# Kernel optimization log

Measured on AMD Instinct MI355X. Metric: run time of the kernel, lower is better.

The kernel has to match this reference:

```python
import jax, jax.numpy as jnp
import numpy as np

DIM = 128; D_STATE = 16; D_CONV = 4; EXPAND = 2
D_INNER = DIM * EXPAND            # 256
DT_RANK = (DIM + 15) // 16        # 8
B, H, W = 2, 56, 56


def _ln(x, w, b):
    m = jnp.mean(x, -1, keepdims=True)
    v = jnp.var(x, -1, keepdims=True)
    return (x - m) * jax.lax.rsqrt(v + 1e-5) * w + b


def _mamba(x, in_w, conv_w, conv_b, xproj_w, dt_w, dt_b, A_log, Dp, out_w):
    # x: (B, L, DIM)
    Bb, L, _ = x.shape
    xz = x @ in_w.T                                   # (B,L,2*D_INNER)
    xi, z = jnp.split(xz, 2, axis=-1)
    # causal depthwise conv1d (pad left d_conv-1, truncate to L)
    xc = jnp.transpose(xi, (0, 2, 1))                 # (B,D_INNER,L)
    xc = jax.lax.conv_general_dilated(
        xc, conv_w, (1,), [(D_CONV - 1, 0)],
        dimension_numbers=('NCH', 'OIH', 'NCH'),
        feature_group_count=D_INNER) + conv_b[None, :, None]
    xs = jax.nn.silu(jnp.transpose(xc, (0, 2, 1)))    # (B,L,D_INNER)
    dbl = xs @ xproj_w.T                              # (B,L,DT_RANK+2*D_STATE)
    dt = jax.nn.softplus(dbl[..., :DT_RANK] @ dt_w.T + dt_b)   # (B,L,D_INNER)
    Bc = dbl[..., DT_RANK:DT_RANK + D_STATE]          # (B,L,D_STATE)
    Cc = dbl[..., DT_RANK + D_STATE:]                 # (B,L,D_STATE)
    A = -jnp.exp(A_log)                               # (D_INNER,D_STATE)
    dA = jnp.exp(dt[..., None] * A)                   # (B,L,D_INNER,D_STATE)
    dBu = (dt * xs)[..., None] * Bc[:, :, None, :]    # (B,L,D_INNER,D_STATE)

    def step(h, inp):
        a, bu, c = inp
        h = a * h + bu                                # (B,D_INNER,D_STATE)
        return h, jnp.einsum('bdn,bn->bd', h, c)

    h0 = jnp.zeros((Bb, D_INNER, D_STATE), x.dtype)
    _, ys = jax.lax.scan(step, h0, (jnp.moveaxis(dA, 1, 0),
                                    jnp.moveaxis(dBu, 1, 0),
                                    jnp.moveaxis(Cc, 1, 0)))
    y = jnp.moveaxis(ys, 0, 1) + xs * Dp              # (B,L,D_INNER)
    y = y * jax.nn.silu(z)
    return y @ out_w.T                                # (B,L,DIM)


def _forward(x, norm_h_w, norm_h_b, norm_v_w, norm_v_b,
             dw_w, dw_b, pw_w, pw_b,
             h_in_w, h_conv_w, h_conv_b, h_xproj_w, h_dt_w, h_dt_b, h_A_log, h_D, h_out_w,
             v_in_w, v_conv_w, v_conv_b, v_xproj_w, v_dt_w, v_dt_b, v_A_log, v_D, v_out_w,
             ca_fc1_w, ca_fc2_w):
    Bb, C, Hh, Ww = x.shape
    # local branch: depthwise 3x3 + GELU + 1x1
    lf = jax.lax.conv_general_dilated(
        x, dw_w, (1, 1), [(1, 1), (1, 1)],
        dimension_numbers=('NCHW', 'OIHW', 'NCHW'),
        feature_group_count=C) + dw_b[None, :, None, None]
    lf = jax.nn.gelu(lf, approximate=False)
    lf = jnp.einsum('bchw,oc->bohw', lf, pw_w[:, :, 0, 0]) + pw_b[None, :, None, None]
    # horizontal scan: row-major tokens
    xh = _ln(x.reshape(Bb, C, Hh * Ww).transpose(0, 2, 1), norm_h_w, norm_h_b)
    oh = _mamba(xh, h_in_w, h_conv_w, h_conv_b, h_xproj_w, h_dt_w, h_dt_b,
                h_A_log, h_D, h_out_w)
    oh = oh.transpose(0, 2, 1).reshape(Bb, C, Hh, Ww)
    # vertical scan: column-major tokens
    xv = _ln(jnp.transpose(x, (0, 1, 3, 2)).reshape(Bb, C, Ww * Hh).transpose(0, 2, 1),
             norm_v_w, norm_v_b)
    ov = _mamba(xv, v_in_w, v_conv_w, v_conv_b, v_xproj_w, v_dt_w, v_dt_b,
                v_A_log, v_D, v_out_w)
    ov = jnp.transpose(ov.transpose(0, 2, 1).reshape(Bb, C, Ww, Hh), (0, 1, 3, 2))
    fused = oh + ov + lf
    # channel attention
    y = jnp.mean(fused, axis=(2, 3))                  # (B,C)
    y = jax.nn.sigmoid(jax.nn.relu(y @ ca_fc1_w.T) @ ca_fc2_w.T)
    return fused * y[:, :, None, None] + x


def setup_inputs() -> dict:
    key = jax.random.key(0)
    ks = iter(jax.random.split(key, 64))
    def nrm(shape, scale):
        return jax.random.normal(next(ks), shape, jnp.float32) * scale
    d = {}
    d['x'] = nrm((B, DIM, H, W), 1.0)
    d['norm_h_w'] = jnp.ones((DIM,), jnp.float32); d['norm_h_b'] = jnp.zeros((DIM,), jnp.float32)
    d['norm_v_w'] = jnp.ones((DIM,), jnp.float32); d['norm_v_b'] = jnp.zeros((DIM,), jnp.float32)
    d['dw_w'] = nrm((DIM, 1, 3, 3), 1.0 / 3.0)
    d['dw_b'] = jnp.zeros((DIM,), jnp.float32)
    d['pw_w'] = nrm((DIM, DIM, 1, 1), DIM ** -0.5)
    d['pw_b'] = jnp.zeros((DIM,), jnp.float32)
    for p in ('h', 'v'):
        d[p + '_in_w'] = nrm((2 * D_INNER, DIM), DIM ** -0.5)
        d[p + '_conv_w'] = nrm((D_INNER, 1, D_CONV), D_CONV ** -0.5)
        d[p + '_conv_b'] = jnp.zeros((D_INNER,), jnp.float32)
        d[p + '_xproj_w'] = nrm((DT_RANK + 2 * D_STATE, D_INNER), D_INNER ** -0.5)
        d[p + '_dt_w'] = nrm((D_INNER, DT_RANK), DT_RANK ** -0.5)
        d[p + '_dt_b'] = jnp.full((D_INNER,), -2.0, jnp.float32)  # small positive dt
        d[p + '_A_log'] = jnp.log(jnp.tile(jnp.arange(1, D_STATE + 1, dtype=jnp.float32), (D_INNER, 1)))
        d[p + '_D'] = jnp.ones((D_INNER,), jnp.float32)
        d[p + '_out_w'] = nrm((DIM, D_INNER), D_INNER ** -0.5)
    d['ca_fc1_w'] = nrm((DIM // 4, DIM), DIM ** -0.5)
    d['ca_fc2_w'] = nrm((DIM, DIM // 4), (DIM // 4) ** -0.5)
    return d


def reference(x, norm_h_w, norm_h_b, norm_v_w, norm_v_b,
              dw_w, dw_b, pw_w, pw_b,
              h_in_w, h_conv_w, h_conv_b, h_xproj_w, h_dt_w, h_dt_b, h_A_log, h_D, h_out_w,
              v_in_w, v_conv_w, v_conv_b, v_xproj_w, v_dt_w, v_dt_b, v_A_log, v_D, v_out_w,
              ca_fc1_w, ca_fc2_w):
    return _forward(x, norm_h_w, norm_h_b, norm_v_w, norm_v_b,
                    dw_w, dw_b, pw_w, pw_b,
                    h_in_w, h_conv_w, h_conv_b, h_xproj_w, h_dt_w, h_dt_b, h_A_log, h_D, h_out_w,
                    v_in_w, v_conv_w, v_conv_b, v_xproj_w, v_dt_w, v_dt_b, v_A_log, v_D, v_out_w,
                    ca_fc1_w, ca_fc2_w)
```

## Files before the change

kernel.cpp:

```cpp
#include <hip/hip_runtime.h>
#include <hip/hip_bf16.h>

typedef __hip_bfloat16 bf16;
__device__ __forceinline__ float b2f(bf16 v){ return __bfloat162float(v); }
__device__ __forceinline__ bf16 f2b(float v){ return __float2bfloat16(v); }

typedef __attribute__((ext_vector_type(8))) short frag_ab;
typedef __attribute__((ext_vector_type(4))) float frag_cd;
typedef __attribute__((ext_vector_type(4))) short short4v;

__device__ __forceinline__ frag_ab ld_frag_2xb64(const bf16* p){
  union { frag_ab f; short4v h[2]; } u;
  u.h[0] = *reinterpret_cast<const short4v*>(p);
  u.h[1] = *reinterpret_cast<const short4v*>(p+4);
  return u.f;
}

__device__ __forceinline__ void st_agent(float* p, float v){
  __hip_atomic_store(p, v, __ATOMIC_RELAXED, __HIP_MEMORY_SCOPE_AGENT);
}
__device__ __forceinline__ float ld_agent(const float* p){
  return __hip_atomic_load(p, __ATOMIC_RELAXED, __HIP_MEMORY_SCOPE_AGENT);
}

#define LLEN 3136
#define BATCH 2
#define NCHUNK 49
#define LC 64

__global__ void k_front(const float* __restrict__ x, const float* __restrict__ dww,
                        const float* __restrict__ dwb, bf16* __restrict__ tmp,
                        const float* nhw_, const float* nhb_, const float* nvw_,
                        const float* nvb_, bf16* __restrict__ xln,
                        float* __restrict__ YMEAN, int* __restrict__ ZCNT,
                        const float* __restrict__ h_inw, const float* __restrict__ v_inw,
                        const float* __restrict__ h_ow,  const float* __restrict__ v_ow,
                        const float* __restrict__ pww,   const float* __restrict__ h_xw,
                        const float* __restrict__ v_xw,
                        bf16* __restrict__ WBIN, bf16* __restrict__ WBOUT,
                        bf16* __restrict__ WBPW, bf16* __restrict__ WBX){
  int blk = blockIdx.x;
  int tid = threadIdx.x;
  if (blk < 1024){
    int bc = blk & 255;
    int seg = blk >> 8;
    int c = bc & 127;
    if (blk == 0){
      if (tid < 256) YMEAN[tid] = 0.f;
      if (tid < 4)   ZCNT[tid] = 0;
    }
    const float* xp = x + (size_t)bc*LLEN;
    __shared__ float sxr[16][60];
    int r0 = seg*14;
    for (int idx = tid; idx < 16*56; idx += 256){
      int rr = idx/56, cc = idx%56;
      int gr = r0 - 1 + rr;
      sxr[rr][cc+1] = (gr >= 0 && gr < 56) ? xp[gr*56+cc] : 0.f;
    }
    if (tid < 16){ sxr[tid][0] = 0.f; sxr[tid][57] = 0.f; }
    float w[9];
    #pragma unroll
    for (int i=0;i<9;i++) w[i] = dww[c*9+i];
    float bias = dwb[c];
    __syncthreads();
    int pstart = seg * 784;
    for (int p = pstart + tid; p < pstart + 784; p += 256){
      int i = p/56, j = p%56;
      int li = i - r0;
      float acc = bias;
      #pragma unroll
      for (int a=0;a<3;a++)
        #pragma unroll
        for (int bb=0;bb<3;bb++)
          acc += w[a*3+bb] * sxr[li+a][j+bb];
      float g = 0.5f*acc*(1.0f + erff(acc*0.70710678118654752f));
      tmp[(size_t)bc*LLEN + p] = f2b(g);
    }
  } else if (blk < 1136){
    int idx2 = blk - 1024;
    int h = idx2 % 56, b = idx2 / 56;
    __shared__ float sx[128][57];
    __shared__ float smean[56], srstd[56];
    __shared__ float wh[128], bh[128], wv_[128], bv_[128];
    if (tid < 128){ wh[tid]=nhw_[tid]; bh[tid]=nhb_[tid];
                    wv_[tid]=nvw_[tid]; bv_[tid]=nvb_[tid]; }
    for (int idx = tid; idx < 128*56; idx += 256){
      int c = idx / 56, w = idx % 56;
      sx[c][w] = x[((size_t)(b*128+c))*LLEN + h*56 + w];
    }
    __syncthreads();
    if (tid < 56){
      float s=0.f, s2=0.f;
      for (int c=0;c<128;c++){ float v = sx[c][tid]; s+=v; s2+=v*v; }
      float m = s*(1.f/128.f);
      float var = s2*(1.f/128.f) - m*m;
      smean[tid]=m; srstd[tid]=rsqrtf(var+1e-5f);
    }
    __syncthreads();
    bf16* outh = xln;
    bf16* outv = xln + (size_t)BATCH*LLEN*128;
    for (int idx = tid; idx < 56*128; idx += 256){
      int w = idx >> 7, c = idx & 127;
      float v = (sx[c][w]-smean[w])*srstd[w];
      outh[((size_t)b*LLEN + h*56 + w)*128 + c] = f2b(v*wh[c]+bh[c]);
      outv[((size_t)b*LLEN + w*56 + h)*128 + c] = f2b(v*wv_[c]+bv_[c]);
    }
  } else {
    int pblk = blk - 1136;
    int t16 = tid*16;
    if (pblk < 32){
      int g = pblk*4096 + t16;
      int dir = g >> 16, off = g & 65535;
      const float* src = (dir ? v_inw : h_inw) + off;
      bf16* dst = WBIN + g;
      #pragma unroll
      for (int r=0;r<4;r++){
        float4 w4 = *reinterpret_cast<const float4*>(src + r*4);
        bf16 t4[4] = {f2b(w4.x), f2b(w4.y), f2b(w4.z), f2b(w4.w)};
        *reinterpret_cast<double*>(dst + r*4) = *reinterpret_cast<double*>(t4);
      }
    } else if (pblk < 48){
      int g = (pblk-32)*4096 + t16;
      int dir = g >> 15, off = g & 32767;
      const float* src = (dir ? v_ow : h_ow) + off;
      bf16* dst = WBOUT + g;
      #pragma unroll
      for (int r=0;r<4;r++){
        float4 w4 = *reinterpret_cast<const float4*>(src + r*4);
        bf16 t4[4] = {f2b(w4.x), f2b(w4.y), f2b(w4.z), f2b(w4.w)};
        *reinterpret_cast<double*>(dst + r*4) = *reinterpret_cast<double*>(t4);
      }
    } else if (pblk < 52){
      int g = (pblk-48)*4096 + t16;
      const float* src = pww + g;
      bf16* dst = WBPW + g;
      #pragma unroll
      for (int r=0;r<4;r++){
        float4 w4 = *reinterpret_cast<const float4*>(src + r*4);
        bf16 t4[4] = {f2b(w4.x), f2b(w4.y), f2b(w4.z), f2b(w4.w)};
        *reinterpret_cast<double*>(dst + r*4) = *reinterpret_cast<double*>(t4);
      }
    } else if (pblk < 58){
      int g = (pblk-52)*4096 + t16;
      int dir = (g >= 12288) ? 1 : 0;
      int off = g - dir*12288;
      int rr = off >> 8, cc = off & 255;
      bf16* dst = WBX + g;
      if (rr < 40){
        const float* src = (dir ? v_xw : h_xw) + rr*256 + cc;
        #pragma unroll
        for (int r=0;r<4;r++){
          float4 w4 = *reinterpret_cast<const float4*>(src + r*4);
          bf16 t4[4] = {f2b(w4.x), f2b(w4.y), f2b(w4.z), f2b(w4.w)};
          *reinterpret_cast<double*>(dst + r*4) = *reinterpret_cast<double*>(t4);
        }
      } else {
        bf16 z4[4] = {f2b(0.f), f2b(0.f), f2b(0.f), f2b(0.f)};
        double zd = *reinterpret_cast<double*>(z4);
        #pragma unroll
        for (int r=0;r<4;r++) *reinterpret_cast<double*>(dst + r*4) = zd;
      }
    }
  }
}

__global__ void k_inproj(const bf16* __restrict__ xln, const bf16* __restrict__ WBIN,
                         bf16* __restrict__ XI, bf16* __restrict__ Z){
  int dir = blockIdx.z;
  const bf16* A = xln + (size_t)dir*BATCH*LLEN*128;
  const bf16* Wb = WBIN + (size_t)dir*512*128;
  int m0 = blockIdx.x*64;
  int npair = blockIdx.y*128;
  __shared__ __align__(16) bf16 sA[64][136];
  __shared__ __align__(16) bf16 sW[64][136];
  int tid = threadIdx.x;
  #pragma unroll
  for (int r=0;r<4;r++){
    int idx = tid + r*256;
    int row = idx >> 4, c8 = (idx & 15)*8;
    *reinterpret_cast<float4*>(&sA[row][c8]) =
        *reinterpret_cast<const float4*>(&A[(size_t)(m0+row)*128 + c8]);
  }
  int wv2 = tid >> 6, lane = tid & 63;
  int qd = lane >> 4, mr = lane & 15;
  bf16* dst = (npair < 256) ? XI : Z;
  int nbase0 = npair & 255;
  size_t dslab = (size_t)dir*BATCH*LLEN*256;
  #pragma unroll
  for (int nt=0; nt<2; nt++){
    int n0 = npair + nt*64;
    __syncthreads();
    #pragma unroll
    for (int r=0;r<4;r++){
      int idx = tid + r*256;
      int row = idx >> 4, c8 = (idx & 15)*8;
      *reinterpret_cast<float4*>(&sW[row][c8]) =
          *reinterpret_cast<const float4*>(&Wb[(size_t)(n0+row)*128 + c8]);
    }
    __syncthreads();
    frag_cd acc[4] = {};
    #pragma unroll
    for (int k0=0;k0<128;k0+=32){
      frag_ab af = *reinterpret_cast<frag_ab*>(&sA[wv2*16+mr][k0+qd*8]);
      #pragma unroll
      for (int t=0;t<4;t++){
        frag_ab bfr = *reinterpret_cast<frag_ab*>(&sW[t*16+mr][k0+qd*8]);
        acc[t] = __builtin_amdgcn_mfma_f32_16x16x32_bf16(af, bfr, acc[t], 0, 0, 0);
      }
    }
    int nb = nbase0 + nt*64;
    #pragma unroll
    for (int t=0;t<4;t++)
      #pragma unroll
      for (int r=0;r<4;r++){
        int row = m0 + wv2*16 + qd*4 + r;
        int col = nb + t*16 + mr;
        dst[dslab + (size_t)row*256 + col] = f2b(acc[t][r]);
      }
  }
}

__global__ void k_dbl(const bf16* __restrict__ XI,
                      const float* hcw, const float* hcb, const float* vcw, const float* vcb,
                      const bf16* __restrict__ WBX,
                      const float* hdw, const float* vdw, const float* hdb, const float* vdb,
                      bf16* __restrict__ XS2, bf16* __restrict__ DT2,
                      float* __restrict__ Bf, float* __restrict__ Cf){
  int m0 = blockIdx.x*64;
  int bd = m0 / LLEN;
  int l0m = m0 % LLEN;
  int dirq = bd >> 1;
  const bf16* XId = XI + (size_t)bd*LLEN*256;
  const bf16* Wb = WBX + (size_t)dirq*48*256;
  const float* cw = dirq ? vcw : hcw;
  const float* cb = dirq ? vcb : hcb;
  __shared__ __align__(16) bf16 sA[67][264];
  __shared__ __align__(16) bf16 sW[48][264];
  __shared__ float sdbl[64][49];
  int tid = threadIdx.x;
  for (int idx = tid; idx < 67*32; idx += 256){
    int row = idx >> 5, c8 = (idx & 31)*8;
    int l = l0m - 3 + row;
    float4 v = make_float4(0.f,0.f,0.f,0.f);
    if (l >= 0) v = *reinterpret_cast<const float4*>(&XId[(size_t)l*256 + c8]);
    *reinterpret_cast<float4*>(&sA[row][c8]) = v;
  }
  #pragma unroll
  for (int r=0;r<6;r++){
    int idx = tid + r*256;
    int row = idx >> 5, c8 = (idx & 31)*8;
    *reinterpret_cast<float4*>(&sW[row][c8]) =
        *reinterpret_cast<const float4*>(&Wb[(size_t)row*256 + c8]);
  }
  __syncthreads();
  {
    float w0=cw[tid*4], w1=cw[tid*4+1], w2=cw[tid*4+2], w3=cw[tid*4+3];
    float cbias = cb[tid];
    size_t x2base = ((size_t)bd*16 + (tid>>4))*LLEN + l0m;
    int c16 = tid & 15;
    float xm3 = b2f(sA[0][tid]), xm2 = b2f(sA[1][tid]), xm1 = b2f(sA[2][tid]);
    #pragma unroll 4
    for (int j=0;j<64;j++){
      float x0 = b2f(sA[j+3][tid]);
      float acc = cbias + w0*xm3 + w1*xm2 + w2*xm1 + w3*x0;
      float s = acc / (1.f + __expf(-acc));
      bf16 sv = f2b(s);
      sA[j][tid] = sv;
      XS2[(x2base + j)*16 + c16] = sv;
      xm3=xm2; xm2=xm1; xm1=x0;
    }
  }
  __syncthreads();
  int wv2 = tid >> 6, lane = tid & 63;
  int qd = lane >> 4, mr = lane & 15;
  frag_cd acc[3] = {};
  #pragma unroll
  for (int k0=0;k0<256;k0+=32){
    frag_ab af = *reinterpret_cast<frag_ab*>(&sA[wv2*16+mr][k0+qd*8]);
    #pragma unroll
    for (int t=0;t<3;t++){
      frag_ab bfr = *reinterpret_cast<frag_ab*>(&sW[t*16+mr][k0+qd*8]);
      acc[t] = __builtin_amdgcn_mfma_f32_16x16x32_bf16(af, bfr, acc[t], 0, 0, 0);
    }
  }
  #pragma unroll
  for (int t=0;t<3;t++)
    #pragma unroll
    for (int r=0;r<4;r++){
      int col = t*16 + mr;
      if (col < 40) sdbl[wv2*16 + qd*4 + r][col] = acc[t][r];
    }
  __syncthreads();
  const float* dtw = dirq ? vdw : hdw;
  const float* dtb = dirq ? vdb : hdb;
  float w8[8];
  #pragma unroll
  for (int r=0;r<8;r++) w8[r] = dtw[tid*8+r];
  float biasv = dtb[tid];
  size_t d2base = ((size_t)bd*16 + (tid>>4))*LLEN + l0m;
  int c16 = tid & 15;
  for (int row=0; row<64; row++){
    float a = biasv;
    #pragma unroll
    for (int r=0;r<8;r++) a += sdbl[row][r]*w8[r];
    float sv = (a > 20.f) ? a : __logf(1.f + __expf(a));
    DT2[(d2base + row)*16 + c16] = f2b(sv);
  }
  #pragma unroll
  for (int r=0;r<8;r++){
    int idx = tid + r*256;
    int row = idx >> 5, o = idx & 31;
    float v = sdbl[row][8+o];
    size_t rr = (size_t)(m0+row)*16;
    if (o < 16) Bf[rr + o] = v;
    else        Cf[rr + (o-16)] = v;
  }
}

__global__ void k_scan1(const bf16* __restrict__ DT2, const bf16* __restrict__ XS2,
                        const float* __restrict__ Bc, const float* hA, const float* vA,
                        float* __restrict__ Pbuf, float* __restrict__ Hbuf){
  int bd = blockIdx.z;
  int g  = blockIdx.y;
  int ck = blockIdx.x;
  int l0 = ck*LC;
  const float* Bd = Bc + (size_t)bd*LLEN*16;
  const float* Alog = (bd >> 1) ? vA : hA;
  int tid = threadIdx.x;
  int dl = tid >> 4, n = tid & 15;
  float A = -__expf(Alog[(g*16+dl)*16+n]);
  __shared__ float sdt[LC][16], sxs[LC][16], sB[LC][16];
  size_t base2 = (((size_t)bd*16 + g)*LLEN + l0)*16;
  #pragma unroll
  for (int r=0;r<4;r++){
    int idx = tid + r*256;
    sdt[idx>>4][idx&15] = b2f(DT2[base2 + idx]);
    sxs[idx>>4][idx&15] = b2f(XS2[base2 + idx]);
    (&sB[0][0])[idx] = Bd[(size_t)l0*16 + idx];
  }
  __syncthreads();
  float h = 0.f, P = 1.f;
  #pragma unroll 8
  for (int i=0;i<LC;i++){
    float a = sdt[i][dl];
    float u = sxs[i][dl];
    float dA = __expf(a * A);
    h = dA*h + (a*u)*sB[i][n];
    P *= dA;
  }
  size_t sidx = (((size_t)bd*16 + g)*NCHUNK + ck)*256 + tid;
  Pbuf[sidx] = P;
  Hbuf[sidx] = h;
}

__global__ void k_scan2(const float* __restrict__ Pbuf, float* __restrict__ Hbuf){
  int q = blockIdx.x;
  int tid = threadIdx.x;
  size_t qb = (size_t)q*NCHUNK*256 + tid;
  float Pv[7], Hv[7];
  float carry = 0.f;
  #pragma unroll
  for (int j=0;j<7;j++){
    Pv[j] = Pbuf[qb + (size_t)j*256];
    Hv[j] = Hbuf[qb + (size_t)j*256];
  }
  #pragma unroll
  for (int b=0;b<7;b++){
    float Pn[7], Hn[7];
    if (b < 6){
      #pragma unroll
      for (int j=0;j<7;j++){
        Pn[j] = Pbuf[qb + (size_t)((b+1)*7+j)*256];
        Hn[j] = Hbuf[qb + (size_t)((b+1)*7+j)*256];
      }
    }
    #pragma unroll
    for (int j=0;j<7;j++){
      Hbuf[qb + (size_t)(b*7+j)*256] = carry;
      carry = Pv[j]*carry + Hv[j];
    }
    if (b < 6){
      #pragma unroll
      for (int j=0;j<7;j++){ Pv[j] = Pn[j]; Hv[j] = Hn[j]; }
    }
  }
}

__global__ void k_scan3(const bf16* __restrict__ DT2, const bf16* __restrict__ XS2,
                        const float* __restrict__ Bc, const float* __restrict__ Cc,
                        const float* hA, const float* vA,
                        const float* __restrict__ Hbuf, bf16* __restrict__ ys){
  int bd = blockIdx.z;
  int g  = blockIdx.y;
  int ck = blockIdx.x;
  int l0 = ck*LC;
  const float* Bd = Bc + (size_t)bd*LLEN*16;
  const float* Cd = Cc + (size_t)bd*LLEN*16;
  bf16* yd = ys + (size_t)bd*LLEN*256;
  const float* Alog = (bd >> 1) ? vA : hA;
  int tid = threadIdx.x;
  int dl = tid >> 4, n = tid & 15;
  float A = -__expf(Alog[(g*16+dl)*16+n]);
  __shared__ float sdt[LC][16], sxs[LC][16], sB[LC][16], sC[LC][16];
  __shared__ float sp2[16][272];
  size_t base2 = (((size_t)bd*16 + g)*LLEN + l0)*16;
  #pragma unroll
  for (int r=0;r<4;r++){
    int idx = tid + r*256;
    sdt[idx>>4][idx&15] = b2f(DT2[base2 + idx]);
    sxs[idx>>4][idx&15] = b2f(XS2[base2 + idx]);
    (&sB[0][0])[idx] = Bd[(size_t)l0*16 + idx];
    (&sC[0][0])[idx] = Cd[(size_t)l0*16 + idx];
  }
  size_t sidx = (((size_t)bd*16 + g)*NCHUNK + ck)*256 + tid;
  float h = Hbuf[sidx];
  __syncthreads();
  int swz = dl*17 + n;
  int i_local = tid >> 4;
  int c16 = tid & 15;
  int rbase = c16*17;
  for (int i0=0; i0<LC; i0+=16){
    #pragma unroll
    for (int ii=0;ii<16;ii++){
      int i = i0 + ii;
      float a = sdt[i][dl];
      float u = sxs[i][dl];
      float dA = __expf(a * A);
      h = dA*h + (a*u)*sB[i][n];
      sp2[ii][swz] = h * sC[i][n];
    }
    __syncthreads();
    const float* row = &sp2[i_local][rbase];
    float s = 0.f;
    #pragma unroll
    for (int k=0;k<16;k++) s += row[k];
    yd[(size_t)(l0+i0+i_local)*256 + g*16 + c16] = f2b(s);
    __syncthreads();
  }
}

__global__ void k_outgemm(const bf16* __restrict__ ys, const bf16* __restrict__ XS2,
                          const bf16* __restrict__ Z, const float* __restrict__ hD,
                          const float* __restrict__ vD, const bf16* __restrict__ WBOUT,
                          bf16* __restrict__ OD){
  int dir = blockIdx.y;
  size_t slab = (size_t)dir*BATCH*LLEN*256;
  const bf16* Wb = WBOUT + (size_t)dir*128*256;
  const float* Dw = dir ? vD : hD;
  bf16* od = OD + (size_t)dir*BATCH*LLEN*128;
  int m0 = blockIdx.x*32;
  int bd = dir*2 + m0/LLEN;
  int lbase = m0 % LLEN;
  __shared__ __align__(16) bf16 sA[32][264];
  __shared__ __align__(16) bf16 sW[64][264];
  int tid = threadIdx.x;
  #pragma unroll
  for (int r=0;r<4;r++){
    int idx = tid + r*256;
    int row = idx >> 5, c8 = (idx & 31)*8;
    size_t e = slab + (size_t)(m0+row)*256 + c8;
    size_t e2 = (((size_t)bd*16 + (c8>>4))*LLEN + lbase + row)*16 + (c8&15);
    bf16 yb[8], xb[8], zb[8], ob[8];
    *reinterpret_cast<float4*>(yb) = *reinterpret_cast<const float4*>(&ys[e]);
    *reinterpret_cast<float4*>(xb) = *reinterpret_cast<const float4*>(&XS2[e2]);
    *reinterpret_cast<float4*>(zb) = *reinterpret_cast<const float4*>(&Z[e]);
    #pragma unroll
    for (int j=0;j<8;j++){
      float Dv = Dw[c8 + j];
      float yv = b2f(yb[j]) + b2f(xb[j])*Dv;
      float zv = b2f(zb[j]);
      ob[j] = f2b(yv * (zv/(1.f+__expf(-zv))));
    }
    *reinterpret_cast<float4*>(&sA[row][c8]) = *reinterpret_cast<float4*>(ob);
  }
  int wv2 = tid >> 6, lane = tid & 63;
  int qd = lane >> 4, mr = lane & 15;
  int msub = wv2 & 1, tpair = (wv2 >> 1)*2;
  #pragma unroll
  for (int nh=0; nh<2; nh++){
    int n0 = nh*64;
    __syncthreads();
    #pragma unroll
    for (int r=0;r<8;r++){
      int idx = tid + r*256;
      int row = idx >> 5, c8 = (idx & 31)*8;
      *reinterpret_cast<float4*>(&sW[row][c8]) =
          *reinterpret_cast<const float4*>(&Wb[(size_t)(n0+row)*256 + c8]);
    }
    __syncthreads();
    frag_cd acc[2] = {};
    #pragma unroll
    for (int k0=0;k0<256;k0+=32){
      frag_ab af = *reinterpret_cast<frag_ab*>(&sA[msub*16+mr][k0+qd*8]);
      #pragma unroll
      for (int i=0;i<2;i++){
        frag_ab bfr = *reinterpret_cast<frag_ab*>(&sW[(tpair+i)*16+mr][k0+qd*8]);
        acc[i] = __builtin_amdgcn_mfma_f32_16x16x32_bf16(af, bfr, acc[i], 0, 0, 0);
      }
    }
    #pragma unroll
    for (int i=0;i<2;i++)
      #pragma unroll
      for (int r=0;r<4;r++){
        int row = m0 + msub*16 + qd*4 + r;
        int col = n0 + (tpair+i)*16 + mr;
        od[(size_t)row*128 + col] = f2b(acc[i][r]);
      }
  }
}

__global__ void k_pwcomb(const bf16* __restrict__ tmp, const bf16* __restrict__ WBPW,
                         const float* __restrict__ pwb, const bf16* __restrict__ OD,
                         const float* __restrict__ x, float* __restrict__ out,
                         float* __restrict__ YMEAN, int* __restrict__ CNTPW,
                         int* __restrict__ FLAG, float* __restrict__ GATE,
                         const float* __restrict__ fc1, const float* __restrict__ fc2){
  int p0 = blockIdx.x * 64;
  int m0 = blockIdx.y * 64;
  int b  = blockIdx.z;
  const bf16* T = tmp + (size_t)b*128*LLEN;
  const bf16* od0 = OD + (size_t)b*LLEN*128;
  const bf16* od1 = OD + (size_t)(BATCH + b)*LLEN*128;
  __shared__ __align__(16) bf16 sA[64][136];
  __shared__ __align__(16) bf16 sBt[64][132];
  __shared__ float sOD[64][65];
  __shared__ float ym[128], s1g[32];
  __shared__ int slast;
  int tid = threadIdx.x;
  #pragma unroll
  for (int r=0;r<4;r++){
    int idx = tid + r*256;
    int row = idx >> 4, c8 = (idx & 15)*8;
    *reinterpret_cast<float4*>(&sA[row][c8]) =
        *reinterpret_cast<const float4*>(&WBPW[(size_t)(m0+row)*128 + c8]);
  }
  #pragma unroll
  for (int r=0;r<8;r++){
    int idx = tid + r*256;
    int c = idx >> 4, p4 = (idx & 15)*4;
    union { double d; bf16 v[4]; } u;
    u.d = *reinterpret_cast<const double*>(&T[(size_t)c*LLEN + p0 + p4]);
    #pragma unroll
    for (int j=0;j<4;j++) sBt[p4+j][c] = u.v[j];
  }
  #pragma unroll
  for (int r=0;r<8;r++){
    int idx = tid + r*256;
    int prow = idx >> 5, mp = (idx & 31)*2;
    int p = p0 + prow;
    int pi = p/56, pj = p%56;
    int pt = pj*56 + pi;
    bf16 a0[2], a1[2];
    *reinterpret_cast<float*>(a0) = *reinterpret_cast<const float*>(&od0[(size_t)p*128 + m0 + mp]);
    *reinterpret_cast<float*>(a1) = *reinterpret_cast<const float*>(&od1[(size_t)pt*128 + m0 + mp]);
    sOD[prow][mp]   = b2f(a0[0]) + b2f(a1[0]);
    sOD[prow][mp+1] = b2f(a0[1]) + b2f(a1[1]);
  }
  __syncthreads();
  int wv2 = tid >> 6, lane = tid & 63;
  int qd = lane >> 4, mr = lane & 15;
  frag_cd acc[4] = {};
  #pragma unroll
  for (int k0=0;k0<128;k0+=32){
    frag_ab af = *reinterpret_cast<frag_ab*>(&sA[wv2*16+mr][k0+qd*8]);
    #pragma unroll
    for (int t=0;t<4;t++){
      frag_ab bfr = ld_frag_2xb64(&sBt[t*16+mr][k0+qd*8]);
      acc[t] = __builtin_amdgcn_mfma_f32_16x16x32_bf16(af, bfr, acc[t], 0, 0, 0);
    }
  }
  float vals[4][4];
  #pragma unroll
  for (int r=0;r<4;r++){
    int m = m0 + wv2*16 + qd*4 + r;
    float bias = pwb[m];
    float s = 0.f;
    #pragma unroll
    for (int t=0;t<4;t++){
      float val = acc[t][r] + bias + sOD[t*16+mr][m - m0];
      vals[t][r] = val;
      s += val;
    }
    s += __shfl_xor(s, 1, 16);
    s += __shfl_xor(s, 2, 16);
    s += __shfl_xor(s, 4, 16);
    s += __shfl_xor(s, 8, 16);
    if (mr == 0) atomicAdd(&YMEAN[b*128 + m], s);
  }
  __syncthreads();
  if (tid == 0) slast = (atomicAdd(&CNTPW[b], 1) == 2*49 - 1);
  __syncthreads();
  if (slast){
    if (tid < 128)
      ym[tid] = ld_agent(&YMEAN[b*128+tid]) * (1.f/(float)LLEN);
    __syncthreads();
    {
      int o = tid >> 3, part = tid & 7;
      float a = 0.f;
      #pragma unroll
      for (int k=0;k<16;k++) a += ym[part*16 + k] * fc1[o*128 + part*16 + k];
      a += __shfl_xor(a, 1, 8);
      a += __shfl_xor(a, 2, 8);
      a += __shfl_xor(a, 4, 8);
      if (part == 0) s1g[o] = fmaxf(a, 0.f);
    }
    __syncthreads();
    if (tid < 128){
      float a = 0.f;
      #pragma unroll
      for (int j=0;j<32;j++) a += s1g[j]*fc2[tid*32+j];
      st_agent(&GATE[b*128+tid], 1.f/(1.f+__expf(-a)));
    }
    __syncthreads();
    if (tid == 0)
      __hip_atomic_store(&FLAG[b], 1, __ATOMIC_RELEASE, __HIP_MEMORY_SCOPE_AGENT);
  } else {
    if (tid == 0)
      while (__hip_atomic_load(&FLAG[b], __ATOMIC_ACQUIRE, __HIP_MEMORY_SCOPE_AGENT) == 0)
        __builtin_amdgcn_s_sleep(2);
  }
  __syncthreads();
  float g4[4];
  #pragma unroll
  for (int r=0;r<4;r++){
    int m = m0 + wv2*16 + qd*4 + r;
    g4[r] = ld_agent(&GATE[b*128+m]);
  }
  #pragma unroll
  for (int t=0;t<4;t++)
    #pragma unroll
    for (int r=0;r<4;r++){
      int m = m0 + wv2*16 + qd*4 + r;
      int p = p0 + t*16 + mr;
      size_t i = ((size_t)b*128 + m)*LLEN + p;
      out[i] = vals[t][r]*g4[r] + x[i];
    }
}

extern "C" void kernel_launch(void* const* d_in, const int* in_sizes, int n_in,
                              void* d_out, int out_size, void* d_ws, size_t ws_size,
                              hipStream_t stream) {
  const float* x      = (const float*)d_in[0];
  const float* nhw    = (const float*)d_in[1];
  const float* nhb    = (const float*)d_in[2];
  const float* nvw    = (const float*)d_in[3];
  const float* nvb    = (const float*)d_in[4];
  const float* dww    = (const float*)d_in[5];
  const float* dwb    = (const float*)d_in[6];
  const float* pww    = (const float*)d_in[7];
  const float* pwb    = (const float*)d_in[8];
  const float* h_inw  = (const float*)d_in[9];
  const float* h_cw   = (const float*)d_in[10];
  const float* h_cb   = (const float*)d_in[11];
  const float* h_xw   = (const float*)d_in[12];
  const float* h_dtw  = (const float*)d_in[13];
  const float* h_dtb  = (const float*)d_in[14];
  const float* h_Al   = (const float*)d_in[15];
  const float* h_D    = (const float*)d_in[16];
  const float* h_ow   = (const float*)d_in[17];
  const float* v_inw  = (const float*)d_in[18];
  const float* v_cw   = (const float*)d_in[19];
  const float* v_cb   = (const float*)d_in[20];
  const float* v_xw   = (const float*)d_in[21];
  const float* v_dtw  = (const float*)d_in[22];
  const float* v_dtb  = (const float*)d_in[23];
  const float* v_Al   = (const float*)d_in[24];
  const float* v_D    = (const float*)d_in[25];
  const float* v_ow   = (const float*)d_in[26];
  const float* fc1    = (const float*)d_in[27];
  const float* fc2    = (const float*)d_in[28];

  float* out = (float*)d_out;

  bf16* WBIN  = (bf16*)((char*)d_out + 0);
  bf16* WBOUT = (bf16*)((char*)d_out + 262144);
  bf16* WBX   = (bf16*)((char*)d_out + 393216);

  char* base = (char*)d_ws;
  bf16*  XLN   = (bf16*)(base + 1605632);
  bf16*  DT2   = (bf16*)(base + 0);
  bf16*  OD    = (bf16*)(base + 0);
  bf16*  XI    = (bf16*)(base + 6422528);
  bf16*  YS    = (bf16*)(base + 6422528);
  bf16*  Z     = (bf16*)(base + 12845056);
  bf16*  XS2   = (bf16*)(base + 19267584);
  float* Bf    = (float*)(base + 25690112);
  float* Cf    = (float*)(base + 26492928);
  float* Hbuf  = (float*)(base + 27295744);
  float* YMEAN = (float*)(base + 30507008);
  bf16*  TMP   = (bf16*)(base + 30508032);
  float* Pbuf  = (float*)(base + 32113664);
  int*   ZCNT  = (int*)  (base + 35324928);
  float* GATE  = (float*)(base + 35325440);
  bf16*  WBPW  = (bf16*) (base + 35326464);
  int*   CNTPW = ZCNT;
  int*   FLAG  = ZCNT + 2;

  k_front<<<dim3(1024 + 56*BATCH + 64), dim3(256), 0, stream>>>(
      x, dww, dwb, TMP, nhw, nhb, nvw, nvb, XLN, YMEAN, ZCNT,
      h_inw, v_inw, h_ow, v_ow, pww, h_xw, v_xw, WBIN, WBOUT, WBPW, WBX);
  k_inproj<<<dim3(98,4,2), dim3(256), 0, stream>>>(XLN, WBIN, XI, Z);
  k_dbl<<<dim3(196), dim3(256), 0, stream>>>(XI, h_cw, h_cb, v_cw, v_cb,
                                             WBX, h_dtw, v_dtw, h_dtb, v_dtb,
                                             XS2, DT2, Bf, Cf);
  k_scan1<<<dim3(NCHUNK,16,4), dim3(256), 0, stream>>>(DT2, XS2, Bf, h_Al, v_Al, Pbuf, Hbuf);
  k_scan2<<<dim3(64), dim3(256), 0, stream>>>(Pbuf, Hbuf);
  k_scan3<<<dim3(NCHUNK,16,4), dim3(256), 0, stream>>>(DT2, XS2, Bf, Cf, h_Al, v_Al, Hbuf, YS);
  k_outgemm<<<dim3(196,2), dim3(256), 0, stream>>>(YS, XS2, Z, h_D, v_D, WBOUT, OD);
  k_pwcomb<<<dim3(49,2,BATCH), dim3(256), 0, stream>>>(TMP, WBPW, pwb, OD, x, out,
                                                       YMEAN, CNTPW, FLAG, GATE, fc1, fc2);
}
```

Before: 220.4 us.

## Compute channel-attention gate from precomputed partial sums instead of in-kernel grid sync

The channel-attention mean of the pointwise-conv output is now derived algebraically: per-channel sums of the depthwise-conv activations (from k_front) are multiplied by the pointwise weights, and column sums of the Mamba output projection (from k_outgemm) are added. A small k_gate kernel then computes the gate, so k_pwcomb no longer needs atomics, a last-block counter or spin-waiting on a flag. This removes the intra-kernel grid-wide synchronization and register-held values in k_pwcomb, at the cost of one extra tiny kernel launch and some extra reductions in earlier kernels. Rounding differs slightly because sums are taken before the bias and GEMM accumulation order changes.

```diff
diff --git a/kernel.cpp b/kernel.cpp
--- a/kernel.cpp
+++ b/kernel.cpp
@@ -16,13 +16,6 @@
   return u.f;
 }
 
-__device__ __forceinline__ void st_agent(float* p, float v){
-  __hip_atomic_store(p, v, __ATOMIC_RELAXED, __HIP_MEMORY_SCOPE_AGENT);
-}
-__device__ __forceinline__ float ld_agent(const float* p){
-  return __hip_atomic_load(p, __ATOMIC_RELAXED, __HIP_MEMORY_SCOPE_AGENT);
-}
-
 #define LLEN 3136
 #define BATCH 2
 #define NCHUNK 49
@@ -32,25 +25,22 @@
                         const float* __restrict__ dwb, bf16* __restrict__ tmp,
                         const float* nhw_, const float* nhb_, const float* nvw_,
                         const float* nvb_, bf16* __restrict__ xln,
-                        float* __restrict__ YMEAN, int* __restrict__ ZCNT,
                         const float* __restrict__ h_inw, const float* __restrict__ v_inw,
                         const float* __restrict__ h_ow,  const float* __restrict__ v_ow,
                         const float* __restrict__ pww,   const float* __restrict__ h_xw,
                         const float* __restrict__ v_xw,
                         bf16* __restrict__ WBIN, bf16* __restrict__ WBOUT,
-                        bf16* __restrict__ WBPW, bf16* __restrict__ WBX){
+                        bf16* __restrict__ WBPW, bf16* __restrict__ WBX,
+                        float* __restrict__ TSUMP){
   int blk = blockIdx.x;
   int tid = threadIdx.x;
   if (blk < 1024){
     int bc = blk & 255;
     int seg = blk >> 8;
     int c = bc & 127;
-    if (blk == 0){
-      if (tid < 256) YMEAN[tid] = 0.f;
-      if (tid < 4)   ZCNT[tid] = 0;
-    }
     const float* xp = x + (size_t)bc*LLEN;
     __shared__ float sxr[16][60];
+    __shared__ float wsum[4];
     int r0 = seg*14;
     for (int idx = tid; idx < 16*56; idx += 256){
       int rr = idx/56, cc = idx%56;
@@ -64,6 +54,7 @@
     float bias = dwb[c];
     __syncthreads();
     int pstart = seg * 784;
+    float ts = 0.f;
     for (int p = pstart + tid; p < pstart + 784; p += 256){
       int i = p/56, j = p%56;
       int li = i - r0;
@@ -74,8 +65,19 @@
         for (int bb=0;bb<3;bb++)
           acc += w[a*3+bb] * sxr[li+a][j+bb];
       float g = 0.5f*acc*(1.0f + erff(acc*0.70710678118654752f));
-      tmp[(size_t)bc*LLEN + p] = f2b(g);
-    }
+      bf16 gb = f2b(g);
+      tmp[(size_t)bc*LLEN + p] = gb;
+      ts += b2f(gb);
+    }
+    ts += __shfl_xor(ts, 1, 64);
+    ts += __shfl_xor(ts, 2, 64);
+    ts += __shfl_xor(ts, 4, 64);
+    ts += __shfl_xor(ts, 8, 64);
+    ts += __shfl_xor(ts, 16, 64);
+    ts += __shfl_xor(ts, 32, 64);
+    if ((tid & 63) == 0) wsum[tid >> 6] = ts;
+    __syncthreads();
+    if (tid == 0) TSUMP[seg*256 + bc] = wsum[0]+wsum[1]+wsum[2]+wsum[3];
   } else if (blk < 1136){
     int idx2 = blk - 1024;
     int h = idx2 % 56, b = idx2 / 56;
@@ -442,7 +444,7 @@
 __global__ void k_outgemm(const bf16* __restrict__ ys, const bf16* __restrict__ XS2,
                           const bf16* __restrict__ Z, const float* __restrict__ hD,
                           const float* __restrict__ vD, const bf16* __restrict__ WBOUT,
-                          bf16* __restrict__ OD){
+                          bf16* __restrict__ OD, float* __restrict__ OSUMP){
   int dir = blockIdx.y;
   size_t slab = (size_t)dir*BATCH*LLEN*256;
   const bf16* Wb = WBOUT + (size_t)dir*128*256;
@@ -453,7 +455,9 @@
   int lbase = m0 % LLEN;
   __shared__ __align__(16) bf16 sA[32][264];
   __shared__ __align__(16) bf16 sW[64][264];
-  int tid = threadIdx.x;
+  __shared__ float scol[128];
+  int tid = threadIdx.x;
+  if (tid < 128) scol[tid] = 0.f;
   #pragma unroll
   for (int r=0;r<4;r++){
     int idx = tid + r*256;
@@ -499,22 +503,75 @@
       }
     }
     #pragma unroll
-    for (int i=0;i<2;i++)
+    for (int i=0;i<2;i++){
+      float cs = 0.f;
       #pragma unroll
       for (int r=0;r<4;r++){
         int row = m0 + msub*16 + qd*4 + r;
         int col = n0 + (tpair+i)*16 + mr;
-        od[(size_t)row*128 + col] = f2b(acc[i][r]);
-      }
+        bf16 ov = f2b(acc[i][r]);
+        od[(size_t)row*128 + col] = ov;
+        cs += b2f(ov);
+      }
+      cs += __shfl_xor(cs, 16, 64);
+      cs += __shfl_xor(cs, 32, 64);
+      if (qd == 0) atomicAdd(&scol[n0 + (tpair+i)*16 + mr], cs);
+    }
+  }
+  __syncthreads();
+  if (tid < 128){
+    int b = m0 / LLEN;
+    int t = blockIdx.x % 98;
+    OSUMP[(((size_t)(dir*2 + b)*98) + t)*128 + tid] = scol[tid];
+  }
+}
+
+__global__ void k_gate(const float* __restrict__ TSUMP, const float* __restrict__ OSUMP,
+                       const bf16* __restrict__ WBPW, const float* __restrict__ pwb,
+                       const float* __restrict__ fc1, const float* __restrict__ fc2,
+                       float* __restrict__ GATE){
+  int b = blockIdx.x;
+  int tid = threadIdx.x;
+  __shared__ float tsh[128], ym[128], s1g[32];
+  if (tid < 128)
+    tsh[tid] = TSUMP[0*256 + b*128 + tid] + TSUMP[1*256 + b*128 + tid]
+             + TSUMP[2*256 + b*128 + tid] + TSUMP[3*256 + b*128 + tid];
+  __syncthreads();
+  if (tid < 128){
+    float os = 0.f;
+    for (int dir=0; dir<2; dir++)
+      for (int t=0; t<98; t++)
+        os += OSUMP[(((size_t)(dir*2 + b)*98) + t)*128 + tid];
+    float pwpart = 0.f;
+    #pragma unroll 8
+    for (int c=0; c<128; c++)
+      pwpart += b2f(WBPW[tid*128 + c]) * tsh[c];
+    ym[tid] = (pwpart + os)*(1.f/(float)LLEN) + pwb[tid];
+  }
+  __syncthreads();
+  {
+    int o = tid >> 3, part = tid & 7;
+    float a = 0.f;
+    #pragma unroll
+    for (int k=0;k<16;k++) a += ym[part*16 + k] * fc1[o*128 + part*16 + k];
+    a += __shfl_xor(a, 1, 8);
+    a += __shfl_xor(a, 2, 8);
+    a += __shfl_xor(a, 4, 8);
+    if (part == 0) s1g[o] = fmaxf(a, 0.f);
+  }
+  __syncthreads();
+  if (tid < 128){
+    float a = 0.f;
+    #pragma unroll
+    for (int j=0;j<32;j++) a += s1g[j]*fc2[tid*32+j];
+    GATE[b*128+tid] = 1.f/(1.f+__expf(-a));
   }
 }
 
 __global__ void k_pwcomb(const bf16* __restrict__ tmp, const bf16* __restrict__ WBPW,
                          const float* __restrict__ pwb, const bf16* __restrict__ OD,
                          const float* __restrict__ x, float* __restrict__ out,
-                         float* __restrict__ YMEAN, int* __restrict__ CNTPW,
-                         int* __restrict__ FLAG, float* __restrict__ GATE,
-                         const float* __restrict__ fc1, const float* __restrict__ fc2){
+                         const float* __restrict__ GATE){
   int p0 = blockIdx.x * 64;
   int m0 = blockIdx.y * 64;
   int b  = blockIdx.z;
@@ -524,8 +581,6 @@
   __shared__ __align__(16) bf16 sA[64][136];
   __shared__ __align__(16) bf16 sBt[64][132];
   __shared__ float sOD[64][65];
-  __shared__ float ym[128], s1g[32];
-  __shared__ int slast;
   int tid = threadIdx.x;
   #pragma unroll
   for (int r=0;r<4;r++){
@@ -569,72 +624,19 @@
       acc[t] = __builtin_amdgcn_mfma_f32_16x16x32_bf16(af, bfr, acc[t], 0, 0, 0);
     }
   }
-  float vals[4][4];
   #pragma unroll
   for (int r=0;r<4;r++){
     int m = m0 + wv2*16 + qd*4 + r;
     float bias = pwb[m];
-    float s = 0.f;
+    float g = GATE[b*128 + m];
     #pragma unroll
     for (int t=0;t<4;t++){
       float val = acc[t][r] + bias + sOD[t*16+mr][m - m0];
-      vals[t][r] = val;
-      s += val;
-    }
-    s += __shfl_xor(s, 1, 16);
-    s += __shfl_xor(s, 2, 16);
-    s += __shfl_xor(s, 4, 16);
-    s += __shfl_xor(s, 8, 16);
-    if (mr == 0) atomicAdd(&YMEAN[b*128 + m], s);
-  }
-  __syncthreads();
-  if (tid == 0) slast = (atomicAdd(&CNTPW[b], 1) == 2*49 - 1);
-  __syncthreads();
-  if (slast){
-    if (tid < 128)
-      ym[tid] = ld_agent(&YMEAN[b*128+tid]) * (1.f/(float)LLEN);
-    __syncthreads();
-    {
-      int o = tid >> 3, part = tid & 7;
-      float a = 0.f;
-      #pragma unroll
-      for (int k=0;k<16;k++) a += ym[part*16 + k] * fc1[o*128 + part*16 + k];
-      a += __shfl_xor(a, 1, 8);
-      a += __shfl_xor(a, 2, 8);
-      a += __shfl_xor(a, 4, 8);
-      if (part == 0) s1g[o] = fmaxf(a, 0.f);
-    }
-    __syncthreads();
-    if (tid < 128){
-      float a = 0.f;
-      #pragma unroll
-      for (int j=0;j<32;j++) a += s1g[j]*fc2[tid*32+j];
-      st_agent(&GATE[b*128+tid], 1.f/(1.f+__expf(-a)));
-    }
-    __syncthreads();
-    if (tid == 0)
-      __hip_atomic_store(&FLAG[b], 1, __ATOMIC_RELEASE, __HIP_MEMORY_SCOPE_AGENT);
-  } else {
-    if (tid == 0)
-      while (__hip_atomic_load(&FLAG[b], __ATOMIC_ACQUIRE, __HIP_MEMORY_SCOPE_AGENT) == 0)
-        __builtin_amdgcn_s_sleep(2);
-  }
-  __syncthreads();
-  float g4[4];
-  #pragma unroll
-  for (int r=0;r<4;r++){
-    int m = m0 + wv2*16 + qd*4 + r;
-    g4[r] = ld_agent(&GATE[b*128+m]);
-  }
-  #pragma unroll
-  for (int t=0;t<4;t++)
-    #pragma unroll
-    for (int r=0;r<4;r++){
-      int m = m0 + wv2*16 + qd*4 + r;
       int p = p0 + t*16 + mr;
       size_t i = ((size_t)b*128 + m)*LLEN + p;
-      out[i] = vals[t][r]*g4[r] + x[i];
-    }
+      out[i] = val*g + x[i];
+    }
+  }
 }
 
 extern "C" void kernel_launch(void* const* d_in, const int* in_sizes, int n_in,
@@ -672,9 +674,11 @@
 
   float* out = (float*)d_out;
 
-  bf16* WBIN  = (bf16*)((char*)d_out + 0);
-  bf16* WBOUT = (bf16*)((char*)d_out + 262144);
-  bf16* WBX   = (bf16*)((char*)d_out + 393216);
+  bf16*  WBIN  = (bf16*) ((char*)d_out + 0);
+  bf16*  WBOUT = (bf16*) ((char*)d_out + 262144);
+  bf16*  WBX   = (bf16*) ((char*)d_out + 393216);
+  float* TSUMP = (float*)((char*)d_out + 442368);
+  float* OSUMP = (float*)((char*)d_out + 446464);
 
   char* base = (char*)d_ws;
   bf16*  XLN   = (bf16*)(base + 1605632);
@@ -687,18 +691,14 @@
   float* Bf    = (float*)(base + 25690112);
   float* Cf    = (float*)(base + 26492928);
   float* Hbuf  = (float*)(base + 27295744);
-  float* YMEAN = (float*)(base + 30507008);
   bf16*  TMP   = (bf16*)(base + 30508032);
   float* Pbuf  = (float*)(base + 32113664);
-  int*   ZCNT  = (int*)  (base + 35324928);
-  float* GATE  = (float*)(base + 35325440);
   bf16*  WBPW  = (bf16*) (base + 35326464);
-  int*   CNTPW = ZCNT;
-  int*   FLAG  = ZCNT + 2;
+  float* GATE  = (float*)(base + 35359232);
 
   k_front<<<dim3(1024 + 56*BATCH + 64), dim3(256), 0, stream>>>(
-      x, dww, dwb, TMP, nhw, nhb, nvw, nvb, XLN, YMEAN, ZCNT,
-      h_inw, v_inw, h_ow, v_ow, pww, h_xw, v_xw, WBIN, WBOUT, WBPW, WBX);
+      x, dww, dwb, TMP, nhw, nhb, nvw, nvb, XLN,
+      h_inw, v_inw, h_ow, v_ow, pww, h_xw, v_xw, WBIN, WBOUT, WBPW, WBX, TSUMP);
   k_inproj<<<dim3(98,4,2), dim3(256), 0, stream>>>(XLN, WBIN, XI, Z);
   k_dbl<<<dim3(196), dim3(256), 0, stream>>>(XI, h_cw, h_cb, v_cw, v_cb,
                                              WBX, h_dtw, v_dtw, h_dtb, v_dtb,
@@ -706,7 +706,7 @@
   k_scan1<<<dim3(NCHUNK,16,4), dim3(256), 0, stream>>>(DT2, XS2, Bf, h_Al, v_Al, Pbuf, Hbuf);
   k_scan2<<<dim3(64), dim3(256), 0, stream>>>(Pbuf, Hbuf);
   k_scan3<<<dim3(NCHUNK,16,4), dim3(256), 0, stream>>>(DT2, XS2, Bf, Cf, h_Al, v_Al, Hbuf, YS);
-  k_outgemm<<<dim3(196,2), dim3(256), 0, stream>>>(YS, XS2, Z, h_D, v_D, WBOUT, OD);
-  k_pwcomb<<<dim3(49,2,BATCH), dim3(256), 0, stream>>>(TMP, WBPW, pwb, OD, x, out,
-                                                       YMEAN, CNTPW, FLAG, GATE, fc1, fc2);
-}
+  k_outgemm<<<dim3(196,2), dim3(256), 0, stream>>>(YS, XS2, Z, h_D, v_D, WBOUT, OD, OSUMP);
+  k_gate<<<dim3(BATCH), dim3(256), 0, stream>>>(TSUMP, OSUMP, WBPW, pwb, fc1, fc2, GATE);
+  k_pwcomb<<<dim3(49,2,BATCH), dim3(256), 0, stream>>>(TMP, WBPW, pwb, OD, x, out, GATE);
+}
```

After: 215.8 us. -2.1%, faster.
